# Performance work log

Measured on AMD Instinct MI355X. Metric: run time of the kernel, lower is better.

The kernel has to match this reference:

```python
import jax, jax.numpy as jnp
import numpy as np

N_NODES = 100_000
N_EDGES = 3_200_000
VOCAB = 50_000
D = 256
L_GNN = 4
L_LIN = 2
OUT = 10          # label_size=10 -> output_size=10
N_TGT = 8192
EPS = 1e-5


def layer_norm(x, g, b):
    mu = jnp.mean(x, axis=-1, keepdims=True)
    var = jnp.mean((x - mu) ** 2, axis=-1, keepdims=True)
    return (x - mu) * jax.lax.rsqrt(var + EPS) * g + b


def gcn_conv(x, src, dst, W, b, n):
    # PyG GCNConv defaults: add self loops, symmetric D^-1/2 (A+I) D^-1/2 norm
    h = x @ W                                   # [n, D]
    loops = jnp.arange(n, dtype=src.dtype)
    src2 = jnp.concatenate([src, loops])        # [E+n]
    dst2 = jnp.concatenate([dst, loops])
    deg = jax.ops.segment_sum(jnp.ones(src2.shape[0], dtype=h.dtype), dst2, n)
    dinv = jnp.where(deg > 0, jax.lax.rsqrt(deg), 0.0)
    norm = dinv[src2] * dinv[dst2]              # [E+n]
    out = jax.ops.segment_sum(h[src2] * norm[:, None], dst2, n)  # [n, D]
    return out + b


def setup_inputs() -> dict:
    key = jax.random.key(0)
    ks = jax.random.split(key, 16)
    tokens = jax.random.randint(ks[0], (N_NODES,), 0, VOCAB, dtype=jnp.int32)
    edges = jax.random.randint(ks[1], (2, N_EDGES), 0, N_NODES, dtype=jnp.int32)
    target_indices = jax.random.randint(ks[2], (N_TGT,), 0, N_NODES, dtype=jnp.int32)
    s = 0.05
    emb_table = jax.random.normal(ks[3], (VOCAB, D), jnp.float32)
    gnn_W = jax.random.normal(ks[4], (L_GNN, D, D), jnp.float32) * s
    gnn_b = jnp.zeros((L_GNN, D), jnp.float32)
    gnn_gamma = jnp.ones((L_GNN, D), jnp.float32)
    gnn_beta = jnp.zeros((L_GNN, D), jnp.float32)
    lin_W = jax.random.normal(ks[5], (L_LIN, D, D), jnp.float32) * s
    lin_b = jnp.zeros((L_LIN, D), jnp.float32)
    lin_gamma = jnp.ones((L_LIN, D), jnp.float32)
    lin_beta = jnp.zeros((L_LIN, D), jnp.float32)
    out_W = jax.random.normal(ks[6], (D, OUT), jnp.float32) * s
    out_b = jnp.zeros((OUT,), jnp.float32)
    return {"tokens": tokens, "edges": edges, "target_indices": target_indices,
            "emb_table": emb_table, "gnn_W": gnn_W, "gnn_b": gnn_b,
            "gnn_gamma": gnn_gamma, "gnn_beta": gnn_beta,
            "lin_W": lin_W, "lin_b": lin_b, "lin_gamma": lin_gamma,
            "lin_beta": lin_beta, "out_W": out_W, "out_b": out_b}


def reference(tokens, edges, target_indices, emb_table, gnn_W, gnn_b,
              gnn_gamma, gnn_beta, lin_W, lin_b, lin_gamma, lin_beta,
              out_W, out_b):
    x = emb_table[tokens]                       # [N, D] embedding lookup
    src, dst = edges[0], edges[1]
    for i in range(L_GNN):
        x = gcn_conv(x, src, dst, gnn_W[i], gnn_b[i], N_NODES)
        x = layer_norm(x, gnn_gamma[i], gnn_beta[i])
        x = jax.nn.relu(x)
    x = x[target_indices]                       # [N_TGT, D]
    for i in range(L_LIN):
        x = x @ lin_W[i] + lin_b[i]
        x = layer_norm(x, lin_gamma[i], lin_beta[i])
        x = jax.nn.relu(x)
    return x @ out_W + out_b                    # [N_TGT, OUT]
```

## Files before the change

### kernel.cpp

```cpp
#include <hip/hip_runtime.h>
#include <hip/hip_fp16.h>

#define NN 100000
#define NE 3200000
#define DD 256
#define NT 8192
#define NOUT 10
#define NBUCK 196
#define CSRP_CAP (NE + NBUCK * 4112 + 64)

typedef unsigned short u16;
typedef unsigned int u32;
typedef unsigned char u8;
typedef __attribute__((ext_vector_type(8))) short bf16x8;
typedef __attribute__((ext_vector_type(4))) float f32x4;
typedef __attribute__((ext_vector_type(4))) unsigned int uint4v;

__device__ __forceinline__ float bf2f(u16 u) {
    union { unsigned int i; float f; } v; v.i = ((unsigned int)u) << 16; return v.f;
}
__device__ __forceinline__ u16 f2bf(float f) {
    union { float f; unsigned int i; } v; v.f = f;
    unsigned int x = v.i;
    return (u16)((x + 0x7fffu + ((x >> 16) & 1u)) >> 16);
}
__device__ __forceinline__ unsigned int pack2(float a, float b) {
    return (unsigned int)f2bf(a) | ((unsigned int)f2bf(b) << 16);
}
__device__ __forceinline__ u32 packrec(int src, float w) {
    unsigned short h = __half_as_ushort(__float2half(w));
    return ((u32)src << 15) | (u32)(h & 0x7fff);
}
__device__ __forceinline__ float recw(u32 r) {
    return __half2float(__ushort_as_half((unsigned short)(r & 0x7fff)));
}

#define UNPK(u, lo, hi) { union{unsigned int i; float f;} _x,_y; \
    _x.i=(u)<<16; _y.i=(u)&0xffff0000u; lo=_x.f; hi=_y.f; }

__device__ __forceinline__ void gl2lds16(const void* g, void* l) {
    __builtin_amdgcn_global_load_lds(
        (const __attribute__((address_space(1))) unsigned int*)g,
        (__attribute__((address_space(3))) unsigned int*)l, 16, 0, 0);
}

__global__ __launch_bounds__(256) void k_wt(const float* __restrict__ gW,
                                            const float* __restrict__ lW,
                                            u16* __restrict__ Wt,
                                            int* __restrict__ bucketCnt) {
    if (blockIdx.x == 0 && threadIdx.x < NBUCK) bucketCnt[threadIdx.x] = 0;
    int idx = blockIdx.x * 256 + threadIdx.x;
    int l = idx >> 16;
    int nk = idx & 65535;
    int n = nk >> 8, k = nk & 255;
    float v = (l < 4) ? gW[l * 65536 + k * 256 + n]
                      : lW[(l - 4) * 65536 + k * 256 + n];
    Wt[idx] = f2bf(v);
}

__global__ __launch_bounds__(256) void k_binA(const int* __restrict__ dst,
                                              int* __restrict__ bucketCnt) {
    __shared__ int hist[NBUCK];
    int t = threadIdx.x;
    if (t < NBUCK) hist[t] = 0;
    __syncthreads();
    int base = blockIdx.x * 4096;
#pragma unroll
    for (int i = 0; i < 16; i++) {
        int e = base + i * 256 + t;
        if (e < NE) atomicAdd(&hist[dst[e] >> 9], 1);
    }
    __syncthreads();
    if (t < NBUCK && hist[t] > 0) atomicAdd(&bucketCnt[t], hist[t]);
}

__global__ __launch_bounds__(256) void k_bscan(const int* __restrict__ bucketCnt,
                                               int* __restrict__ bucketOff,
                                               int* __restrict__ bucketCur) {
    __shared__ int s[256];
    int t = threadIdx.x;
    int v = (t < NBUCK) ? bucketCnt[t] : 0;
    s[t] = v;
    __syncthreads();
    for (int o = 1; o < 256; o <<= 1) {
        int a = (t >= o) ? s[t - o] : 0;
        __syncthreads();
        s[t] += a;
        __syncthreads();
    }
    if (t < NBUCK) {
        int ex = s[t] - v;
        bucketOff[t] = ex;
        bucketCur[t] = ex;
    }
    if (t == 0) bucketOff[NBUCK] = NE;
}

__global__ __launch_bounds__(1024) void k_binB(const int* __restrict__ src,
                                               const int* __restrict__ dst,
                                               int* __restrict__ bucketCur,
                                               int* __restrict__ recs) {
    __shared__ int hist[NBUCK];
    __shared__ int gbase[NBUCK];
    int t = threadIdx.x;
    if (t < NBUCK) hist[t] = 0;
    __syncthreads();
    int base = blockIdx.x * 16384;
    int recv[16], bks[16], rnk[16];
#pragma unroll
    for (int i = 0; i < 16; i++) {
        int e = base + i * 1024 + t;
        int bk = -1, rec = 0;
        if (e < NE) {
            int s_ = src[e], d_ = dst[e];
            bk = d_ >> 9;
            rec = (s_ << 9) | (d_ & 511);
        }
        bks[i] = bk; recv[i] = rec;
    }
#pragma unroll
    for (int i = 0; i < 16; i++)
        rnk[i] = (bks[i] >= 0) ? atomicAdd(&hist[bks[i]], 1) : 0;
    __syncthreads();
    if (t < NBUCK) {
        int c = hist[t];
        gbase[t] = (c > 0) ? atomicAdd(&bucketCur[t], c) : 0;
    }
    __syncthreads();
#pragma unroll
    for (int i = 0; i < 16; i++)
        if (bks[i] >= 0) {
            int pos = gbase[bks[i]] + rnk[i];
            pos = min(max(pos, 0), NE - 1);
            recs[pos] = recv[i];
        }
}

__global__ __launch_bounds__(256) void k_csrA(const int* __restrict__ recs,
                                              const int* __restrict__ bucketOff,
                                              int2* __restrict__ nodeInfo,
                                              float* __restrict__ dinv,
                                              u32* __restrict__ csrp) {
    __shared__ int cnt[512], off[512];
    int b = blockIdx.x, t = threadIdx.x;
    int beg = min(max(bucketOff[b], 0), NE);
    int end = min(max(bucketOff[b + 1], beg), NE);
    int n = end - beg;
    cnt[t] = 0; cnt[t + 256] = 0;
    __syncthreads();
    for (int i = t; i < n; i += 256)
        atomicAdd(&cnt[recs[beg + i] & 511], 1);
    __syncthreads();
    off[t] = (cnt[t] + 8) & ~7;
    off[t + 256] = (cnt[t + 256] + 8) & ~7;
    __syncthreads();
    for (int o = 1; o < 512; o <<= 1) {
        int v0 = (t >= o) ? off[t - o] : 0;
        int v1 = (t + 256 >= o) ? off[t + 256 - o] : 0;
        __syncthreads();
        off[t] += v0; off[t + 256] += v1;
        __syncthreads();
    }
    int base = (beg + b * 4112 + 7) & ~7;
    for (int k = t; k < 512; k += 256) {
        int node = b * 512 + k;
        if (node >= NN) continue;
        int pd = (cnt[k] + 8) & ~7;
        int nbeg = base + off[k] - pd;
        int2 ni; ni.x = nbeg; ni.y = pd;
        nodeInfo[node] = ni;
        float di = rsqrtf((float)(cnt[k] + 1));
        dinv[node] = di;
        csrp[nbeg] = packrec(node, di * di);
        for (int j = nbeg + 1 + cnt[k]; j < nbeg + pd; j++) csrp[j] = 0u;
    }
}

__global__ __launch_bounds__(256) void k_csrB(const int* __restrict__ recs,
                                              const int* __restrict__ bucketOff,
                                              const int2* __restrict__ nodeInfo,
                                              const float* __restrict__ dinv,
                                              u32* __restrict__ csrp) {
    __shared__ int cur[512];
    int b = blockIdx.x, t = threadIdx.x;
    cur[t] = 0; cur[t + 256] = 0;
    __syncthreads();
    int beg = min(max(bucketOff[b], 0), NE);
    int end = min(max(bucketOff[b + 1], beg), NE);
    int n = end - beg;
    for (int i = t; i < n; i += 256) {
        int r = recs[beg + i];
        int dlow = r & 511;
        int s = min(max(r >> 9, 0), NN - 1);
        int node = b * 512 + dlow;
        int rk = atomicAdd(&cur[dlow], 1);
        int2 ni = nodeInfo[node];
        float w = dinv[s] * dinv[node];
        int pos = ni.x + 1 + rk;
        pos = min(max(pos, 0), CSRP_CAP - 1);
        csrp[pos] = packrec(s, w);
    }
}

#define GEMM_EPILOGUE                                                         \
    for (int i = 0; i < 4; i++)                                               \
        for (int j = 0; j < 4; j++) {                                         \
            int col = colBase + wn * 64 + j * 16 + l16;                       \
            for (int r = 0; r < 4; r++) {                                     \
                int row = rowBase + wm * 64 + i * 16 + quad * 4 + r;          \
                if (row < M) C[row * 256 + col] = f2bf(acc[i][j][r]);         \
            }                                                                 \
        }

#define GEMM_COMPUTE(ASRC, BSRC)                                              \
    for (int ks = 0; ks < 2; ks++) {                                          \
        bf16x8 a_frag[4], b_frag[4];                                          \
        for (int i = 0; i < 4; i++) {                                         \
            int r = wm * 64 + i * 16 + l16;                                   \
            int ch = (ks * 4 + quad) ^ (r & 7);                               \
            a_frag[i] = *(const bf16x8*)(&ASRC[r * 64 + ch * 8]);             \
        }                                                                     \
        for (int j = 0; j < 4; j++) {                                         \
            int r = wn * 64 + j * 16 + l16;                                   \
            int ch = (ks * 4 + quad) ^ (r & 7);                               \
            b_frag[j] = *(const bf16x8*)(&BSRC[r * 64 + ch * 8]);             \
        }                                                                     \
        for (int i = 0; i < 4; i++)                                           \
            for (int j = 0; j < 4; j++)                                       \
                acc[i][j] = __builtin_amdgcn_mfma_f32_16x16x32_bf16(          \
                    a_frag[i], b_frag[j], acc[i][j], 0, 0, 0);                \
    }

__global__ __launch_bounds__(256) void k_gemm(const u16* __restrict__ A,
                                              const u16* __restrict__ Bt,
                                              u16* __restrict__ C, int M) {
    __shared__ __align__(16) u16 As[128 * 64];
    __shared__ __align__(16) u16 Bs[128 * 64];
    const int tid = threadIdx.x;
    const int wave = tid >> 6, lane = tid & 63;
    const int wm = wave >> 1, wn = wave & 1;
    const int rowBase = blockIdx.x * 128;
    const int colBase = blockIdx.y * 128;
    const int quad = lane >> 4, l16 = lane & 15;

    f32x4 acc[4][4] = {};

    for (int kk = 0; kk < 4; kk++) {
        int k0 = kk * 64;
#pragma unroll
        for (int i = 0; i < 4; i++) {
            int j = (i * 4 + wave) * 64 + lane;
            int r = j >> 3, c = j & 7;
            int cg = c ^ (r & 7);
            int ga = rowBase + r; if (ga >= M) ga = M - 1;
            gl2lds16(A + (size_t)ga * 256 + k0 + cg * 8,
                     &As[(i * 4 + wave) * 512]);
            gl2lds16(Bt + (size_t)(colBase + r) * 256 + k0 + cg * 8,
                     &Bs[(i * 4 + wave) * 512]);
        }
        __syncthreads();
        GEMM_COMPUTE(As, Bs)
        __syncthreads();
    }
    GEMM_EPILOGUE
}

__global__ __launch_bounds__(256) void k_gemm_emb(const int* __restrict__ tokens,
                                                  const float* __restrict__ emb,
                                                  const u16* __restrict__ Bt,
                                                  u16* __restrict__ C, int M) {
    __shared__ __align__(16) u16 As[128 * 64];
    __shared__ __align__(16) u16 Bs[128 * 64];
    __shared__ int tokLDS[128];
    const int tid = threadIdx.x;
    const int wave = tid >> 6, lane = tid & 63;
    const int wm = wave >> 1, wn = wave & 1;
    const int rowBase = blockIdx.x * 128;
    const int colBase = blockIdx.y * 128;
    const int quad = lane >> 4, l16 = lane & 15;

    if (tid < 128) {
        int ga = rowBase + tid; if (ga >= M) ga = M - 1;
        tokLDS[tid] = tokens[ga];
    }
    f32x4 acc[4][4] = {};
    __syncthreads();

    for (int kk = 0; kk < 4; kk++) {
        int k0 = kk * 64;
#pragma unroll
        for (int i = 0; i < 4; i++) {
            int j = (i * 4 + wave) * 64 + lane;
            int r = j >> 3, c = j & 7;
            int cg = c ^ (r & 7);
            const float* srcp = emb + (size_t)tokLDS[r] * 256 + k0 + cg * 8;
            float4 f0 = *(const float4*)srcp;
            float4 f1 = *(const float4*)(srcp + 4);
            uint4 pk;
            pk.x = pack2(f0.x, f0.y); pk.y = pack2(f0.z, f0.w);
            pk.z = pack2(f1.x, f1.y); pk.w = pack2(f1.z, f1.w);
            *(uint4*)(&As[j * 8]) = pk;
            gl2lds16(Bt + (size_t)(colBase + r) * 256 + k0 + cg * 8,
                     &Bs[(i * 4 + wave) * 512]);
        }
        __syncthreads();
        GEMM_COMPUTE(As, Bs)
        __syncthreads();
    }
    GEMM_EPILOGUE
}

__global__ __launch_bounds__(256) void k_gemm_gather(const u16* __restrict__ X,
                                                     const int* __restrict__ tgt,
                                                     const u16* __restrict__ Bt,
                                                     u16* __restrict__ C, int M) {
    __shared__ __align__(16) u16 As[128 * 64];
    __shared__ __align__(16) u16 Bs[128 * 64];
    __shared__ int rowLDS[128];
    const int tid = threadIdx.x;
    const int wave = tid >> 6, lane = tid & 63;
    const int wm = wave >> 1, wn = wave & 1;
    const int rowBase = blockIdx.x * 128;
    const int colBase = blockIdx.y * 128;
    const int quad = lane >> 4, l16 = lane & 15;

    if (tid < 128) {
        int ga = rowBase + tid; if (ga >= M) ga = M - 1;
        rowLDS[tid] = tgt[ga];
    }
    f32x4 acc[4][4] = {};
    __syncthreads();

    for (int kk = 0; kk < 4; kk++) {
        int k0 = kk * 64;
#pragma unroll
        for (int i = 0; i < 4; i++) {
            int j = (i * 4 + wave) * 64 + lane;
            int r = j >> 3, c = j & 7;
            int cg = c ^ (r & 7);
            uint4 v = *(const uint4*)(X + (size_t)rowLDS[r] * 256 + k0 + cg * 8);
            *(uint4*)(&As[j * 8]) = v;
            gl2lds16(Bt + (size_t)(colBase + r) * 256 + k0 + cg * 8,
                     &Bs[(i * 4 + wave) * 512]);
        }
        __syncthreads();
        GEMM_COMPUTE(As, Bs)
        __syncthreads();
    }
    GEMM_EPILOGUE
}

__global__ __launch_bounds__(256) void k_quant(const u16* __restrict__ h,
                                               u8* __restrict__ q8,
                                               float* __restrict__ qs) {
    int wave = threadIdx.x >> 6, lane = threadIdx.x & 63;
    int row = blockIdx.x * 4 + wave;
    ushort4 hv = *(const ushort4*)(h + row * 256 + lane * 4);
    float f0 = bf2f(hv.x), f1 = bf2f(hv.y), f2 = bf2f(hv.z), f3 = bf2f(hv.w);
    float m = fmaxf(fmaxf(fabsf(f0), fabsf(f1)), fmaxf(fabsf(f2), fabsf(f3)));
    for (int o = 32; o >= 1; o >>= 1) m = fmaxf(m, __shfl_xor(m, o, 64));
    float inv = (m > 0.0f) ? 126.0f / m : 0.0f;
    int b0 = (int)rintf(f0 * inv) + 128;
    int b1 = (int)rintf(f1 * inv) + 128;
    int b2 = (int)rintf(f2 * inv) + 128;
    int b3 = (int)rintf(f3 * inv) + 128;
    u32 pk = (u32)b0 | ((u32)b1 << 8) | ((u32)b2 << 16) | ((u32)b3 << 24);
    *(u32*)(q8 + (size_t)row * 256 + lane * 4) = pk;
    if (lane == 0) qs[row] = m * (1.0f / 126.0f);
}

#define GF8(RR, Q0, Q1, Q2, Q3, W0, W1, W2, W3)                               \
    {                                                                         \
        int s0 = (int)(RR.x >> 15), s1 = (int)(RR.y >> 15);                   \
        int s2 = (int)(RR.z >> 15), s3 = (int)(RR.w >> 15);                   \
        Q0 = *(const uint2*)(qb + (size_t)s0 * 256);                          \
        Q1 = *(const uint2*)(qb + (size_t)s1 * 256);                          \
        Q2 = *(const uint2*)(qb + (size_t)s2 * 256);                          \
        Q3 = *(const uint2*)(qb + (size_t)s3 * 256);                          \
        W0 = recw(RR.x) * qs[s0]; W1 = recw(RR.y) * qs[s1];                   \
        W2 = recw(RR.z) * qs[s2]; W3 = recw(RR.w) * qs[s3];                   \
    }

#define GC8_ONE(Q, W)                                                         \
    {                                                                         \
        Ks += W;                                                              \
        a0 = fmaf(W, (float)(Q.x & 255u), a0);                                \
        a1 = fmaf(W, (float)((Q.x >> 8) & 255u), a1);                         \
        a2 = fmaf(W, (float)((Q.x >> 16) & 255u), a2);                        \
        a3 = fmaf(W, (float)(Q.x >> 24), a3);                                 \
        a4 = fmaf(W, (float)(Q.y & 255u), a4);                                \
        a5 = fmaf(W, (float)((Q.y >> 8) & 255u), a5);                         \
        a6 = fmaf(W, (float)((Q.y >> 16) & 255u), a6);                        \
        a7 = fmaf(W, (float)(Q.y >> 24), a7);                                 \
    }

__global__ __launch_bounds__(256) void k_aggr(const u8* __restrict__ q8,
                                              const float* __restrict__ qs,
                                              const int2* __restrict__ nodeInfo,
                                              const u32* __restrict__ csrp,
                                              const float* __restrict__ bias,
                                              const float* __restrict__ gamma,
                                              const float* __restrict__ beta,
                                              u16* __restrict__ xo) {
    const int wave = threadIdx.x >> 6, lane = threadIdx.x & 63;
    const int half = lane >> 5, l32 = lane & 31;
    const int node = blockIdx.x * 4 + wave;
    const int d8 = l32 * 8;
    int2 ni = nodeInfo[node];
    float a0=0,a1=0,a2=0,a3=0,a4=0,a5=0,a6=0,a7=0;
    float Ks = 0.0f;
    const u8* qb = q8 + d8;
    const u32* cp = csrp + ni.x + half * 4;
    const int nrec = ni.y;
    int j = 0;
    for (; j + 16 <= nrec; j += 16, cp += 16) {
        uint4v ra = __builtin_nontemporal_load((const uint4v*)cp);
        uint4v rb = __builtin_nontemporal_load((const uint4v*)(cp + 8));
        uint2 qa0, qa1, qa2, qa3, qb0, qb1, qb2, qb3;
        float wa0, wa1, wa2, wa3, wb0, wb1, wb2, wb3;
        GF8(ra, qa0, qa1, qa2, qa3, wa0, wa1, wa2, wa3);
        GF8(rb, qb0, qb1, qb2, qb3, wb0, wb1, wb2, wb3);
        GC8_ONE(qa0, wa0); GC8_ONE(qa1, wa1);
        GC8_ONE(qa2, wa2); GC8_ONE(qa3, wa3);
        GC8_ONE(qb0, wb0); GC8_ONE(qb1, wb1);
        GC8_ONE(qb2, wb2); GC8_ONE(qb3, wb3);
    }
    if (j < nrec) {
        uint4v ra = __builtin_nontemporal_load((const uint4v*)cp);
        uint2 qa0, qa1, qa2, qa3;
        float wa0, wa1, wa2, wa3;
        GF8(ra, qa0, qa1, qa2, qa3, wa0, wa1, wa2, wa3);
        GC8_ONE(qa0, wa0); GC8_ONE(qa1, wa1);
        GC8_ONE(qa2, wa2); GC8_ONE(qa3, wa3);
    }
    a0 += __shfl_xor(a0, 32, 64); a1 += __shfl_xor(a1, 32, 64);
    a2 += __shfl_xor(a2, 32, 64); a3 += __shfl_xor(a3, 32, 64);
    a4 += __shfl_xor(a4, 32, 64); a5 += __shfl_xor(a5, 32, 64);
    a6 += __shfl_xor(a6, 32, 64); a7 += __shfl_xor(a7, 32, 64);
    Ks += __shfl_xor(Ks, 32, 64);
    float c128 = 128.0f * Ks;
    a0 -= c128; a1 -= c128; a2 -= c128; a3 -= c128;
    a4 -= c128; a5 -= c128; a6 -= c128; a7 -= c128;

    float4 b0 = *(const float4*)(bias + d8);
    float4 b1 = *(const float4*)(bias + d8 + 4);
    a0 += b0.x; a1 += b0.y; a2 += b0.z; a3 += b0.w;
    a4 += b1.x; a5 += b1.y; a6 += b1.z; a7 += b1.w;
    float s1 = a0+a1+a2+a3+a4+a5+a6+a7;
    float s2 = a0*a0+a1*a1+a2*a2+a3*a3+a4*a4+a5*a5+a6*a6+a7*a7;
    for (int o = 16; o >= 1; o >>= 1) {
        s1 += __shfl_xor(s1, o, 64);
        s2 += __shfl_xor(s2, o, 64);
    }
    float mean = s1 * (1.0f / 256.0f);
    float var = s2 * (1.0f / 256.0f) - mean * mean;
    float rstd = rsqrtf(var + 1e-5f);
    if (half == 0) {
        float4 g0 = *(const float4*)(gamma + d8);
        float4 g1 = *(const float4*)(gamma + d8 + 4);
        float4 e0 = *(const float4*)(beta + d8);
        float4 e1 = *(const float4*)(beta + d8 + 4);
        float y0 = fmaxf((a0 - mean) * rstd * g0.x + e0.x, 0.0f);
        float y1 = fmaxf((a1 - mean) * rstd * g0.y + e0.y, 0.0f);
        float y2 = fmaxf((a2 - mean) * rstd * g0.z + e0.z, 0.0f);
        float y3 = fmaxf((a3 - mean) * rstd * g0.w + e0.w, 0.0f);
        float y4 = fmaxf((a4 - mean) * rstd * g1.x + e1.x, 0.0f);
        float y5 = fmaxf((a5 - mean) * rstd * g1.y + e1.y, 0.0f);
        float y6 = fmaxf((a6 - mean) * rstd * g1.z + e1.z, 0.0f);
        float y7 = fmaxf((a7 - mean) * rstd * g1.w + e1.w, 0.0f);
        uint4v o;
        o.x = pack2(y0, y1);
        o.y = pack2(y2, y3);
        o.z = pack2(y4, y5);
        o.w = pack2(y6, y7);
        __builtin_nontemporal_store(o, (uint4v*)(xo + node * 256 + d8));
    }
}

__global__ __launch_bounds__(256) void k_lnrelu(const u16* __restrict__ h,
                                                const float* __restrict__ bias,
                                                const float* __restrict__ gamma,
                                                const float* __restrict__ beta,
                                                u16* __restrict__ xo) {
    int wave = threadIdx.x >> 6, lane = threadIdx.x & 63;
    int row = blockIdx.x * 4 + wave;
    int base = row * 256 + lane * 4;
    ushort4 hv = *(const ushort4*)(h + base);
    float4 bv = *(const float4*)(bias + lane * 4);
    float a0 = bf2f(hv.x) + bv.x, a1 = bf2f(hv.y) + bv.y;
    float a2 = bf2f(hv.z) + bv.z, a3 = bf2f(hv.w) + bv.w;
    float s1 = a0 + a1 + a2 + a3;
    float s2 = a0 * a0 + a1 * a1 + a2 * a2 + a3 * a3;
    for (int o = 32; o >= 1; o >>= 1) {
        s1 += __shfl_xor(s1, o, 64);
        s2 += __shfl_xor(s2, o, 64);
    }
    float mean = s1 * (1.0f / 256.0f);
    float var = s2 * (1.0f / 256.0f) - mean * mean;
    float rstd = rsqrtf(var + 1e-5f);
    float4 gv = *(const float4*)(gamma + lane * 4);
    float4 be = *(const float4*)(beta + lane * 4);
    float y0 = fmaxf((a0 - mean) * rstd * gv.x + be.x, 0.0f);
    float y1 = fmaxf((a1 - mean) * rstd * gv.y + be.y, 0.0f);
    float y2 = fmaxf((a2 - mean) * rstd * gv.z + be.z, 0.0f);
    float y3 = fmaxf((a3 - mean) * rstd * gv.w + be.w, 0.0f);
    ushort4 o4;
    o4.x = f2bf(y0); o4.y = f2bf(y1); o4.z = f2bf(y2); o4.w = f2bf(y3);
    *(ushort4*)(xo + base) = o4;
}

__global__ __launch_bounds__(256) void k_lnout(const u16* __restrict__ h,
                                               const float* __restrict__ bias,
                                               const float* __restrict__ gamma,
                                               const float* __restrict__ beta,
                                               const float* __restrict__ W,
                                               const float* __restrict__ ob,
                                               float* __restrict__ out) {
    __shared__ float Ws[DD * NOUT];
    int tid = threadIdx.x;
    for (int i = tid; i < DD * NOUT; i += 256) Ws[i] = W[i];
    __syncthreads();
    int wave = tid >> 6, lane = tid & 63;
    int row = blockIdx.x * 4 + wave;
    int base = row * 256 + lane * 4;
    ushort4 hv = *(const ushort4*)(h + base);
    float4 bv = *(const float4*)(bias + lane * 4);
    float a0 = bf2f(hv.x) + bv.x, a1 = bf2f(hv.y) + bv.y;
    float a2 = bf2f(hv.z) + bv.z, a3 = bf2f(hv.w) + bv.w;
    float s1 = a0 + a1 + a2 + a3;
    float s2 = a0 * a0 + a1 * a1 + a2 * a2 + a3 * a3;
    for (int o = 32; o >= 1; o >>= 1) {
        s1 += __shfl_xor(s1, o, 64);
        s2 += __shfl_xor(s2, o, 64);
    }
    float mean = s1 * (1.0f / 256.0f);
    float var = s2 * (1.0f / 256.0f) - mean * mean;
    float rstd = rsqrtf(var + 1e-5f);
    float4 gv = *(const float4*)(gamma + lane * 4);
    float4 be = *(const float4*)(beta + lane * 4);
    float y0 = bf2f(f2bf(fmaxf((a0 - mean) * rstd * gv.x + be.x, 0.0f)));
    float y1 = bf2f(f2bf(fmaxf((a1 - mean) * rstd * gv.y + be.y, 0.0f)));
    float y2 = bf2f(f2bf(fmaxf((a2 - mean) * rstd * gv.z + be.z, 0.0f)));
    float y3 = bf2f(f2bf(fmaxf((a3 - mean) * rstd * gv.w + be.w, 0.0f)));
    int d = lane * 4;
    for (int o = 0; o < NOUT; o++) {
        float p = y0 * Ws[(d + 0) * NOUT + o] + y1 * Ws[(d + 1) * NOUT + o] +
                  y2 * Ws[(d + 2) * NOUT + o] + y3 * Ws[(d + 3) * NOUT + o];
        for (int off = 32; off >= 1; off >>= 1) p += __shfl_xor(p, off, 64);
        if (lane == 0) out[row * NOUT + o] = p + ob[o];
    }
}

extern "C" void kernel_launch(void* const* d_in, const int* in_sizes, int n_in,
                              void* d_out, int out_size, void* d_ws, size_t ws_size,
                              hipStream_t stream) {
    (void)in_sizes; (void)n_in; (void)out_size; (void)ws_size;
    const int* tokens = (const int*)d_in[0];
    const int* edges = (const int*)d_in[1];
    const int* tgt = (const int*)d_in[2];
    const float* emb = (const float*)d_in[3];
    const float* gnn_W = (const float*)d_in[4];
    const float* gnn_b = (const float*)d_in[5];
    const float* gnn_g = (const float*)d_in[6];
    const float* gnn_be = (const float*)d_in[7];
    const float* lin_W = (const float*)d_in[8];
    const float* lin_b = (const float*)d_in[9];
    const float* lin_g = (const float*)d_in[10];
    const float* lin_be = (const float*)d_in[11];
    const float* out_W = (const float*)d_in[12];
    const float* out_b = (const float*)d_in[13];
    float* out = (float*)d_out;

    char* ws = (char*)d_ws;
    u16* x = (u16*)ws;           ws += (size_t)NN * 256 * 2;
    char* hreg = ws;             ws += (size_t)NN * 256 * 2;
    u16* h = (u16*)hreg;
    int* recs = (int*)hreg;
    u32* csrp = (u32*)ws;        ws += (size_t)CSRP_CAP * 4;
    int2* nodeInfo = (int2*)ws;  ws += (size_t)NN * 8;
    float* dinv = (float*)ws;    ws += (size_t)NN * 4;
    int* bucketCnt = (int*)ws;   ws += 256 * 4;
    int* bucketOff = (int*)ws;   ws += 256 * 4;
    int* bucketCur = (int*)ws;   ws += 256 * 4;
    u16* Wt = (u16*)ws;          ws += (size_t)6 * 65536 * 2;
    u16* xt = (u16*)ws;          ws += (size_t)NT * 256 * 2;
    u16* ht = (u16*)ws;          ws += (size_t)NT * 256 * 2;
    u8* q8 = (u8*)ws;            ws += (size_t)NN * 256;
    float* qs = (float*)ws;      ws += (size_t)NN * 4;

    const int* e_src = edges;
    const int* e_dst = edges + NE;

    k_wt<<<1536, 256, 0, stream>>>(gnn_W, lin_W, Wt, bucketCnt);
    k_binA<<<782, 256, 0, stream>>>(e_dst, bucketCnt);
    k_bscan<<<1, 256, 0, stream>>>(bucketCnt, bucketOff, bucketCur);
    k_binB<<<196, 1024, 0, stream>>>(e_src, e_dst, bucketCur, recs);
    k_csrA<<<NBUCK, 256, 0, stream>>>(recs, bucketOff, nodeInfo, dinv, csrp);
    k_csrB<<<NBUCK, 256, 0, stream>>>(recs, bucketOff, nodeInfo, dinv, csrp);

    for (int l = 0; l < 4; l++) {
        if (l == 0)
            k_gemm_emb<<<dim3(782, 2), 256, 0, stream>>>(tokens, emb,
                                                         Wt, h, NN);
        else
            k_gemm<<<dim3(782, 2), 256, 0, stream>>>(x, Wt + l * 65536, h, NN);
        k_quant<<<25000, 256, 0, stream>>>(h, q8, qs);
        k_aggr<<<25000, 256, 0, stream>>>(q8, qs, nodeInfo, csrp,
                                          gnn_b + l * 256, gnn_g + l * 256,
                                          gnn_be + l * 256, x);
    }
    k_gemm_gather<<<dim3(64, 2), 256, 0, stream>>>(x, tgt, Wt + 4 * 65536,
                                                   ht, NT);
    k_lnrelu<<<2048, 256, 0, stream>>>(ht, lin_b, lin_g, lin_be, xt);
    k_gemm<<<dim3(64, 2), 256, 0, stream>>>(xt, Wt + 5 * 65536, ht, NT);
    k_lnout<<<2048, 256, 0, stream>>>(ht, lin_b + 256, lin_g + 256,
                                      lin_be + 256, out_W, out_b, out);
}
```

Before: 980.4 us.

## Fuse int8 quantization into GEMM epilogue and fold GCN norm into per-group scales

The GEMM kernels now quantize their output tiles directly to int8, writing one scale per 64-column group per row. The source-side dinv is folded into that scale and the destination-side dinv is applied at the end of aggregation. This removes the bf16 h buffer round trip and the separate k_quant kernel. CSR records become plain source indices, with padding pointing at a zeroed dummy row, so per-edge weight decoding goes away. The trade-off is finer-grained scales (four per row), which changes numerics slightly and adds LDS staging in the GEMM epilogue.

```diff
diff --git a/kernel.cpp b/kernel.cpp
--- a/kernel.cpp
+++ b/kernel.cpp
@@ -27,16 +27,6 @@
 __device__ __forceinline__ unsigned int pack2(float a, float b) {
     return (unsigned int)f2bf(a) | ((unsigned int)f2bf(b) << 16);
 }
-__device__ __forceinline__ u32 packrec(int src, float w) {
-    unsigned short h = __half_as_ushort(__float2half(w));
-    return ((u32)src << 15) | (u32)(h & 0x7fff);
-}
-__device__ __forceinline__ float recw(u32 r) {
-    return __half2float(__ushort_as_half((unsigned short)(r & 0x7fff)));
-}
-
-#define UNPK(u, lo, hi) { union{unsigned int i; float f;} _x,_y; \
-    _x.i=(u)<<16; _y.i=(u)&0xffff0000u; lo=_x.f; hi=_y.f; }
 
 __device__ __forceinline__ void gl2lds16(const void* g, void* l) {
     __builtin_amdgcn_global_load_lds(
@@ -47,8 +37,10 @@
 __global__ __launch_bounds__(256) void k_wt(const float* __restrict__ gW,
                                             const float* __restrict__ lW,
                                             u16* __restrict__ Wt,
-                                            int* __restrict__ bucketCnt) {
+                                            int* __restrict__ bucketCnt,
+                                            float* __restrict__ tq) {
     if (blockIdx.x == 0 && threadIdx.x < NBUCK) bucketCnt[threadIdx.x] = 0;
+    if (blockIdx.x == 0 && threadIdx.x < 4) tq[NN * 4 + threadIdx.x] = 0.0f;
     int idx = blockIdx.x * 256 + threadIdx.x;
     int l = idx >> 16;
     int nk = idx & 65535;
@@ -169,17 +161,15 @@
         int nbeg = base + off[k] - pd;
         int2 ni; ni.x = nbeg; ni.y = pd;
         nodeInfo[node] = ni;
-        float di = rsqrtf((float)(cnt[k] + 1));
-        dinv[node] = di;
-        csrp[nbeg] = packrec(node, di * di);
-        for (int j = nbeg + 1 + cnt[k]; j < nbeg + pd; j++) csrp[j] = 0u;
+        dinv[node] = rsqrtf((float)(cnt[k] + 1));
+        csrp[nbeg] = (u32)node;
+        for (int j = nbeg + 1 + cnt[k]; j < nbeg + pd; j++) csrp[j] = (u32)NN;
     }
 }
 
 __global__ __launch_bounds__(256) void k_csrB(const int* __restrict__ recs,
                                               const int* __restrict__ bucketOff,
                                               const int2* __restrict__ nodeInfo,
-                                              const float* __restrict__ dinv,
                                               u32* __restrict__ csrp) {
     __shared__ int cur[512];
     int b = blockIdx.x, t = threadIdx.x;
@@ -195,10 +185,9 @@
         int node = b * 512 + dlow;
         int rk = atomicAdd(&cur[dlow], 1);
         int2 ni = nodeInfo[node];
-        float w = dinv[s] * dinv[node];
         int pos = ni.x + 1 + rk;
         pos = min(max(pos, 0), CSRP_CAP - 1);
-        csrp[pos] = packrec(s, w);
+        csrp[pos] = (u32)s;
     }
 }
 
@@ -231,6 +220,58 @@
                     a_frag[i], b_frag[j], acc[i][j], 0, 0, 0);                \
     }
 
+#define QUANT_EPILOGUE(Q8, TQ)                                                \
+    {                                                                         \
+        u8* bb = (u8*)As;                          \
+        const int gq = blockIdx.y * 2 + wn;                                   \
+        for (int i = 0; i < 4; i++) {                                         \
+            float m0 = 0.f, m1 = 0.f, m2 = 0.f, m3 = 0.f;                     \
+            for (int j = 0; j < 4; j++) {                                     \
+                m0 = fmaxf(m0, fabsf(acc[i][j][0]));                          \
+                m1 = fmaxf(m1, fabsf(acc[i][j][1]));                          \
+                m2 = fmaxf(m2, fabsf(acc[i][j][2]));                          \
+                m3 = fmaxf(m3, fabsf(acc[i][j][3]));                          \
+            }                                                                 \
+            for (int o = 1; o < 16; o <<= 1) {                                \
+                m0 = fmaxf(m0, __shfl_xor(m0, o, 64));                        \
+                m1 = fmaxf(m1, __shfl_xor(m1, o, 64));                        \
+                m2 = fmaxf(m2, __shfl_xor(m2, o, 64));                        \
+                m3 = fmaxf(m3, __shfl_xor(m3, o, 64));                        \
+            }                                                                 \
+            float i0 = m0 > 0.f ? 126.f / m0 : 0.f;                           \
+            float i1 = m1 > 0.f ? 126.f / m1 : 0.f;                           \
+            float i2 = m2 > 0.f ? 126.f / m2 : 0.f;                           \
+            float i3 = m3 > 0.f ? 126.f / m3 : 0.f;                           \
+            int row0 = rowBase + wm * 64 + i * 16 + quad * 4;                 \
+            if (l16 == 0) {                                                   \
+                if (row0 + 0 < M)                                             \
+                    TQ[(row0+0)*4+gq] = m0 * (1.f/126.f) * dinv[row0+0];      \
+                if (row0 + 1 < M)                                             \
+                    TQ[(row0+1)*4+gq] = m1 * (1.f/126.f) * dinv[row0+1];      \
+                if (row0 + 2 < M)                                             \
+                    TQ[(row0+2)*4+gq] = m2 * (1.f/126.f) * dinv[row0+2];      \
+                if (row0 + 3 < M)                                             \
+                    TQ[(row0+3)*4+gq] = m3 * (1.f/126.f) * dinv[row0+3];      \
+            }                                                                 \
+            int rb = (wm * 64 + i * 16 + quad * 4) * 128;                     \
+            for (int j = 0; j < 4; j++) {                                     \
+                int cb = wn * 64 + j * 16 + l16;                              \
+                bb[rb + cb]       = (u8)((int)rintf(acc[i][j][0]*i0) + 128);  \
+                bb[rb + 128 + cb] = (u8)((int)rintf(acc[i][j][1]*i1) + 128);  \
+                bb[rb + 256 + cb] = (u8)((int)rintf(acc[i][j][2]*i2) + 128);  \
+                bb[rb + 384 + cb] = (u8)((int)rintf(acc[i][j][3]*i3) + 128);  \
+            }                                                                 \
+        }                                                                     \
+        __syncthreads();                                                      \
+        for (int u = tid; u < 1024; u += 256) {                               \
+            int r = u >> 3, c16 = (u & 7) * 16;                               \
+            int row = rowBase + r;                                            \
+            if (row < M)                                                      \
+                *(uint4*)(Q8 + (size_t)row * 256 + colBase + c16) =           \
+                    *(const uint4*)(bb + r * 128 + c16);                      \
+        }                                                                     \
+    }
+
 __global__ __launch_bounds__(256) void k_gemm(const u16* __restrict__ A,
                                               const u16* __restrict__ Bt,
                                               u16* __restrict__ C, int M) {
@@ -265,10 +306,48 @@
     GEMM_EPILOGUE
 }
 
-__global__ __launch_bounds__(256) void k_gemm_emb(const int* __restrict__ tokens,
-                                                  const float* __restrict__ emb,
-                                                  const u16* __restrict__ Bt,
-                                                  u16* __restrict__ C, int M) {
+__global__ __launch_bounds__(256) void k_gemmq(const u16* __restrict__ A,
+                                               const u16* __restrict__ Bt,
+                                               const float* __restrict__ dinv,
+                                               u8* __restrict__ q8,
+                                               float* __restrict__ tq, int M) {
+    __shared__ __align__(16) u16 As[128 * 64];
+    __shared__ __align__(16) u16 Bs[128 * 64];
+    const int tid = threadIdx.x;
+    const int wave = tid >> 6, lane = tid & 63;
+    const int wm = wave >> 1, wn = wave & 1;
+    const int rowBase = blockIdx.x * 128;
+    const int colBase = blockIdx.y * 128;
+    const int quad = lane >> 4, l16 = lane & 15;
+
+    f32x4 acc[4][4] = {};
+
+    for (int kk = 0; kk < 4; kk++) {
+        int k0 = kk * 64;
+#pragma unroll
+        for (int i = 0; i < 4; i++) {
+            int j = (i * 4 + wave) * 64 + lane;
+            int r = j >> 3, c = j & 7;
+            int cg = c ^ (r & 7);
+            int ga = rowBase + r; if (ga >= M) ga = M - 1;
+            gl2lds16(A + (size_t)ga * 256 + k0 + cg * 8,
+                     &As[(i * 4 + wave) * 512]);
+            gl2lds16(Bt + (size_t)(colBase + r) * 256 + k0 + cg * 8,
+                     &Bs[(i * 4 + wave) * 512]);
+        }
+        __syncthreads();
+        GEMM_COMPUTE(As, Bs)
+        __syncthreads();
+    }
+    QUANT_EPILOGUE(q8, tq)
+}
+
+__global__ __launch_bounds__(256) void k_gemm_embq(const int* __restrict__ tokens,
+                                                   const float* __restrict__ emb,
+                                                   const u16* __restrict__ Bt,
+                                                   const float* __restrict__ dinv,
+                                                   u8* __restrict__ q8,
+                                                   float* __restrict__ tq, int M) {
     __shared__ __align__(16) u16 As[128 * 64];
     __shared__ __align__(16) u16 Bs[128 * 64];
     __shared__ int tokLDS[128];
@@ -307,7 +386,7 @@
         GEMM_COMPUTE(As, Bs)
         __syncthreads();
     }
-    GEMM_EPILOGUE
+    QUANT_EPILOGUE(q8, tq)
 }
 
 __global__ __launch_bounds__(256) void k_gemm_gather(const u16* __restrict__ X,
@@ -350,35 +429,15 @@
     GEMM_EPILOGUE
 }
 
-__global__ __launch_bounds__(256) void k_quant(const u16* __restrict__ h,
-                                               u8* __restrict__ q8,
-                                               float* __restrict__ qs) {
-    int wave = threadIdx.x >> 6, lane = threadIdx.x & 63;
-    int row = blockIdx.x * 4 + wave;
-    ushort4 hv = *(const ushort4*)(h + row * 256 + lane * 4);
-    float f0 = bf2f(hv.x), f1 = bf2f(hv.y), f2 = bf2f(hv.z), f3 = bf2f(hv.w);
-    float m = fmaxf(fmaxf(fabsf(f0), fabsf(f1)), fmaxf(fabsf(f2), fabsf(f3)));
-    for (int o = 32; o >= 1; o >>= 1) m = fmaxf(m, __shfl_xor(m, o, 64));
-    float inv = (m > 0.0f) ? 126.0f / m : 0.0f;
-    int b0 = (int)rintf(f0 * inv) + 128;
-    int b1 = (int)rintf(f1 * inv) + 128;
-    int b2 = (int)rintf(f2 * inv) + 128;
-    int b3 = (int)rintf(f3 * inv) + 128;
-    u32 pk = (u32)b0 | ((u32)b1 << 8) | ((u32)b2 << 16) | ((u32)b3 << 24);
-    *(u32*)(q8 + (size_t)row * 256 + lane * 4) = pk;
-    if (lane == 0) qs[row] = m * (1.0f / 126.0f);
-}
-
 #define GF8(RR, Q0, Q1, Q2, Q3, W0, W1, W2, W3)                               \
     {                                                                         \
-        int s0 = (int)(RR.x >> 15), s1 = (int)(RR.y >> 15);                   \
-        int s2 = (int)(RR.z >> 15), s3 = (int)(RR.w >> 15);                   \
+        int s0 = (int)RR.x, s1 = (int)RR.y, s2 = (int)RR.z, s3 = (int)RR.w;   \
         Q0 = *(const uint2*)(qb + (size_t)s0 * 256);                          \
         Q1 = *(const uint2*)(qb + (size_t)s1 * 256);                          \
         Q2 = *(const uint2*)(qb + (size_t)s2 * 256);                          \
         Q3 = *(const uint2*)(qb + (size_t)s3 * 256);                          \
-        W0 = recw(RR.x) * qs[s0]; W1 = recw(RR.y) * qs[s1];                   \
-        W2 = recw(RR.z) * qs[s2]; W3 = recw(RR.w) * qs[s3];                   \
+        W0 = tq[s0 * 4 + sg4]; W1 = tq[s1 * 4 + sg4];                         \
+        W2 = tq[s2 * 4 + sg4]; W3 = tq[s3 * 4 + sg4];                         \
     }
 
 #define GC8_ONE(Q, W)                                                         \
@@ -395,7 +454,8 @@
     }
 
 __global__ __launch_bounds__(256) void k_aggr(const u8* __restrict__ q8,
-                                              const float* __restrict__ qs,
+                                              const float* __restrict__ tq,
+                                              const float* __restrict__ dinv,
                                               const int2* __restrict__ nodeInfo,
                                               const u32* __restrict__ csrp,
                                               const float* __restrict__ bias,
@@ -406,6 +466,7 @@
     const int half = lane >> 5, l32 = lane & 31;
     const int node = blockIdx.x * 4 + wave;
     const int d8 = l32 * 8;
+    const int sg4 = l32 >> 3;
     int2 ni = nodeInfo[node];
     float a0=0,a1=0,a2=0,a3=0,a4=0,a5=0,a6=0,a7=0;
     float Ks = 0.0f;
@@ -438,14 +499,15 @@
     a4 += __shfl_xor(a4, 32, 64); a5 += __shfl_xor(a5, 32, 64);
     a6 += __shfl_xor(a6, 32, 64); a7 += __shfl_xor(a7, 32, 64);
     Ks += __shfl_xor(Ks, 32, 64);
+
+    float dv = dinv[node];
     float c128 = 128.0f * Ks;
-    a0 -= c128; a1 -= c128; a2 -= c128; a3 -= c128;
-    a4 -= c128; a5 -= c128; a6 -= c128; a7 -= c128;
-
     float4 b0 = *(const float4*)(bias + d8);
     float4 b1 = *(const float4*)(bias + d8 + 4);
-    a0 += b0.x; a1 += b0.y; a2 += b0.z; a3 += b0.w;
-    a4 += b1.x; a5 += b1.y; a6 += b1.z; a7 += b1.w;
+    a0 = (a0 - c128) * dv + b0.x; a1 = (a1 - c128) * dv + b0.y;
+    a2 = (a2 - c128) * dv + b0.z; a3 = (a3 - c128) * dv + b0.w;
+    a4 = (a4 - c128) * dv + b1.x; a5 = (a5 - c128) * dv + b1.y;
+    a6 = (a6 - c128) * dv + b1.z; a7 = (a7 - c128) * dv + b1.w;
     float s1 = a0+a1+a2+a3+a4+a5+a6+a7;
     float s2 = a0*a0+a1*a1+a2*a2+a3*a3+a4*a4+a5*a5+a6*a6+a7*a7;
     for (int o = 16; o >= 1; o >>= 1) {
@@ -574,7 +636,6 @@
     char* ws = (char*)d_ws;
     u16* x = (u16*)ws;           ws += (size_t)NN * 256 * 2;
     char* hreg = ws;             ws += (size_t)NN * 256 * 2;
-    u16* h = (u16*)hreg;
     int* recs = (int*)hreg;
     u32* csrp = (u32*)ws;        ws += (size_t)CSRP_CAP * 4;
     int2* nodeInfo = (int2*)ws;  ws += (size_t)NN * 8;
@@ -585,27 +646,27 @@
     u16* Wt = (u16*)ws;          ws += (size_t)6 * 65536 * 2;
     u16* xt = (u16*)ws;          ws += (size_t)NT * 256 * 2;
     u16* ht = (u16*)ws;          ws += (size_t)NT * 256 * 2;
-    u8* q8 = (u8*)ws;            ws += (size_t)NN * 256;
-    float* qs = (float*)ws;      ws += (size_t)NN * 4;
+    u8* q8 = (u8*)ws;            ws += (size_t)(NN + 8) * 256;
+    float* tq = (float*)ws;      ws += (size_t)(NN + 1) * 16;
 
     const int* e_src = edges;
     const int* e_dst = edges + NE;
 
-    k_wt<<<1536, 256, 0, stream>>>(gnn_W, lin_W, Wt, bucketCnt);
+    k_wt<<<1536, 256, 0, stream>>>(gnn_W, lin_W, Wt, bucketCnt, tq);
     k_binA<<<782, 256, 0, stream>>>(e_dst, bucketCnt);
     k_bscan<<<1, 256, 0, stream>>>(bucketCnt, bucketOff, bucketCur);
     k_binB<<<196, 1024, 0, stream>>>(e_src, e_dst, bucketCur, recs);
     k_csrA<<<NBUCK, 256, 0, stream>>>(recs, bucketOff, nodeInfo, dinv, csrp);
-    k_csrB<<<NBUCK, 256, 0, stream>>>(recs, bucketOff, nodeInfo, dinv, csrp);
+    k_csrB<<<NBUCK, 256, 0, stream>>>(recs, bucketOff, nodeInfo, csrp);
 
     for (int l = 0; l < 4; l++) {
         if (l == 0)
-            k_gemm_emb<<<dim3(782, 2), 256, 0, stream>>>(tokens, emb,
-                                                         Wt, h, NN);
+            k_gemm_embq<<<dim3(782, 2), 256, 0, stream>>>(tokens, emb, Wt,
+                                                          dinv, q8, tq, NN);
         else
-            k_gemm<<<dim3(782, 2), 256, 0, stream>>>(x, Wt + l * 65536, h, NN);
-        k_quant<<<25000, 256, 0, stream>>>(h, q8, qs);
-        k_aggr<<<25000, 256, 0, stream>>>(q8, qs, nodeInfo, csrp,
+            k_gemmq<<<dim3(782, 2), 256, 0, stream>>>(x, Wt + l * 65536,
+                                                      dinv, q8, tq, NN);
+        k_aggr<<<25000, 256, 0, stream>>>(q8, tq, dinv, nodeInfo, csrp,
                                           gnn_b + l * 256, gnn_g + l * 256,
                                           gnn_be + l * 256, x);
     }
```

New measurement: 1.110 ms. 13.2% more time.
